# Kernel optimization log

Measured on AMD Instinct MI355X. Metric: run time of the kernel, lower is better.

## Reference

```python
import jax, jax.numpy as jnp
import numpy as np

MAX_REL = 127  # default max_relative_position of NEZHA-style RelativePositionsEncoding


def rel_pos_encoding(L, d):
    """Clipped relative-distance sinusoidal encoding, shape [L, L, d]."""
    vocab = 2 * MAX_REL + 1
    pos = np.arange(vocab, dtype=np.float32)[:, None]
    i = np.arange(d)
    div = np.power(10000.0, (2 * (i // 2)) / d).astype(np.float32)
    ang = pos / div
    table = np.where(i % 2 == 0, np.sin(ang), np.cos(ang)).astype(np.float32)  # [vocab, d]
    dist = np.clip(np.arange(L)[None, :] - np.arange(L)[:, None], -MAX_REL, MAX_REL) + MAX_REL
    return jnp.asarray(table[dist])  # [L, L, d]


def setup_inputs() -> dict:
    key = jax.random.key(0)
    ks = jax.random.split(key, 5)
    B, L, H, C = 2, 256, 256, 5
    return {
        "hidden_state": jax.random.normal(ks[0], (B, L, H), dtype=jnp.float32),
        "mask": jnp.ones((B, L), dtype=jnp.int32),
        "Wh_w": jax.random.normal(ks[1], (4 * H, H), dtype=jnp.float32) * 0.02,
        "Wh_b": jax.random.normal(ks[2], (H,), dtype=jnp.float32) * 0.02,
        "Wo_w": jax.random.normal(ks[3], (H, C), dtype=jnp.float32) * 0.02,
        "Wo_b": jax.random.normal(ks[4], (C,), dtype=jnp.float32) * 0.02,
    }


def reference(hidden_state, mask, Wh_w, Wh_b, Wo_w, Wo_b):
    B, L, H = hidden_state.shape
    # Decompose Wh over the concat [end, start, end-start, end*start]:
    # Wh(cat) = end@(We+Wd) + start@(Ws-Wd) + (end*start)@Wm + rel@Wh + b  (exact, linearity)
    We, Ws, Wd, Wm = jnp.split(Wh_w, 4, axis=0)  # each [H, H]
    rel = rel_pos_encoding(L, 4 * H)                        # [L, L, 4H]
    rel_term = jnp.einsum('ijk,kh->ijh', rel, Wh_w)         # [L, L, H]
    a = hidden_state @ (We + Wd)                            # end-index contribution  [B, L, H]
    b = hidden_state @ (Ws - Wd)                            # start-index contribution [B, L, H]
    prod = hidden_state[:, :, None, :] * hidden_state[:, None, :, :]  # [B, L, L, H]
    pre = a[:, :, None, :] + b[:, None, :, :] + prod @ Wm + rel_term[None] + Wh_b
    hij = jnp.tanh(pre)                                     # [B, L, L, H]
    logits = hij @ Wo_w + Wo_b                              # [B, L, L, C]
    logits = jnp.transpose(logits, (0, 3, 1, 2))            # [B, C, L, L]
    m = mask.astype(bool)
    bad = (~m[:, None, :, None]) | (~m[:, None, None, :])
    logits = jnp.where(bad, -jnp.inf, logits)
    tri = jnp.tril(jnp.ones((L, L), logits.dtype), -1) * 1e12
    return logits - tri
```

## Files before the change

kernel.cpp:

```cpp
#include <hip/hip_runtime.h>
#include <math.h>

typedef _Float16 half8 __attribute__((ext_vector_type(8)));
typedef _Float16 half4v __attribute__((ext_vector_type(4)));
typedef float floatx4 __attribute__((ext_vector_type(4)));

union U16 { uint4 u; half8 h; };

__global__ __launch_bounds__(256) void k_prep1(
    const float* __restrict__ hs, const float* __restrict__ Wh,
    const float* __restrict__ Wo,
    float* __restrict__ Rp, float* __restrict__ ap, float* __restrict__ bp,
    uint4* __restrict__ WmT2, uint4* __restrict__ WoPk)
{
  __shared__ __align__(16) char pool[32768];
  int bid = blockIdx.x, tid = threadIdx.x;

  if (bid < 256) {
    float (*tbl)[8] = (float(*)[8])pool;
    int dg = bid >> 3, kq = bid & 7, d0 = dg * 8, k0 = kq * 128;
    for (int idx = tid; idx < 1024; idx += 256) {
      int t = idx >> 3, dl = idx & 7;
      int k = k0 + t;
      float e = (float)(k & ~1) * (1.0f / 1024.f);
      float div = powf(10000.f, e);
      float ang = (float)(d0 + dl) / div;
      tbl[t][dl] = (k & 1) ? cosf(ang) : sinf(ang);
    }
    __syncthreads();
    int h = tid;
    float acc[8] = {0, 0, 0, 0, 0, 0, 0, 0};
    for (int kk = 0; kk < 128; ++kk) {
      float wv = Wh[(k0 + kk) * 256 + h];
      float tr[8];
      *(float4*)&tr[0] = *(const float4*)&tbl[kk][0];
      *(float4*)&tr[4] = *(const float4*)&tbl[kk][4];
#pragma unroll
      for (int dl = 0; dl < 8; ++dl) acc[dl] = fmaf(tr[dl], wv, acc[dl]);
    }
#pragma unroll
    for (int dl = 0; dl < 8; ++dl)
      Rp[kq * 65536 + (d0 + dl) * 256 + h] = acc[dl];

  } else if (bid < 512) {
    float (*xs)[8] = (float(*)[8])pool;
    int g = bid - 256, rg = g >> 2, kq = g & 3;
    int r0 = rg * 8, k0 = kq * 64;
    for (int idx = tid; idx < 512; idx += 256) {
      int kk = idx >> 3, r = idx & 7;
      xs[kk][r] = hs[(r0 + r) * 256 + k0 + kk];
    }
    __syncthreads();
    int h = tid;
    float aa[8] = {0, 0, 0, 0, 0, 0, 0, 0}, bb[8] = {0, 0, 0, 0, 0, 0, 0, 0};
    for (int kk = 0; kk < 64; ++kk) {
      int k = k0 + kk;
      float we = Wh[k * 256 + h];
      float wsv = Wh[(256 + k) * 256 + h];
      float wd = Wh[(512 + k) * 256 + h];
      float wA = we + wd, wB = wsv - wd;
      float xr[8];
      *(float4*)&xr[0] = *(const float4*)&xs[kk][0];
      *(float4*)&xr[4] = *(const float4*)&xs[kk][4];
#pragma unroll
      for (int r = 0; r < 8; ++r) {
        aa[r] = fmaf(xr[r], wA, aa[r]);
        bb[r] = fmaf(xr[r], wB, bb[r]);
      }
    }
#pragma unroll
    for (int r = 0; r < 8; ++r) {
      ap[kq * 131072 + (r0 + r) * 256 + h] = aa[r];
      bp[kq * 131072 + (r0 + r) * 256 + h] = bb[r];
    }

  } else if (bid < 516) {
    _Float16 (*T)[256] = (_Float16(*)[256])pool;
    int q = bid - 512;
    for (int idx = tid; idx < 16384; idx += 256) {
      int k = idx >> 8, h = idx & 255;
      T[k][h] = (_Float16)Wh[(768 + q * 64 + k) * 256 + h];
    }
    __syncthreads();
    for (int gi = tid; gi < 2048; gi += 256) {
      int kbl = gi >> 8, h = gi & 255;
      U16 v;
#pragma unroll
      for (int e = 0; e < 8; ++e) v.h[e] = T[kbl * 8 + e][h];
      WmT2[(q * 8 + kbl) * 256 + h] = v.u;
    }

  } else {
    for (int gi = tid; gi < 512; gi += 256) {
      int kb = gi >> 4, c = gi & 15;
      U16 v;
#pragma unroll
      for (int e = 0; e < 8; ++e)
        v.h[e] = (c < 5) ? (_Float16)Wo[(kb * 8 + e) * 5 + c] : (_Float16)0.f;
      WoPk[gi] = v.u;
    }
  }
}

__global__ __launch_bounds__(256) void k_prep2(
    const float* __restrict__ Rp, const float* __restrict__ ap,
    const float* __restrict__ bp,
    float* __restrict__ R, float* __restrict__ a, float* __restrict__ bv)
{
  int bid = blockIdx.x, h = threadIdx.x;
  if (bid < 255) {
    int d = bid;
    float s = 0.f;
#pragma unroll
    for (int kq = 0; kq < 8; ++kq) s += Rp[kq * 65536 + d * 256 + h];
    R[d * 256 + h] = s;
  } else {
    int r0 = (bid - 255) * 2;
#pragma unroll
    for (int rr = 0; rr < 2; ++rr) {
      int r = r0 + rr;
      float sa = 0.f, sb = 0.f;
#pragma unroll
      for (int kq = 0; kq < 4; ++kq) {
        sa += ap[kq * 131072 + r * 256 + h];
        sb += bp[kq * 131072 + r * 256 + h];
      }
      a[r * 256 + h] = sa;
      bv[r * 256 + h] = sb;
    }
  }
}

__global__ __launch_bounds__(256, 5) void k_main(
    const float* __restrict__ hs, const int* __restrict__ mask,
    const float* __restrict__ R, const float* __restrict__ a,
    const float* __restrict__ bvec, const float* __restrict__ Whb,
    const uint4* __restrict__ WmT2, const uint4* __restrict__ WoPk,
    const float* __restrict__ Wob, float* __restrict__ out)
{
  __shared__ __align__(16) _Float16 As[32][264];

  int bid = blockIdx.x, tid = threadIdx.x;
  int jt = bid & 7, i = (bid >> 3) & 255, b = bid >> 11;
  int j0 = jt * 32;
  int lane = tid & 63, w = tid >> 6;
  int c16 = lane & 15, quad = lane >> 4;
  const float* hsb = hs + (size_t)b * 65536;

  float av[4];
#pragma unroll
  for (int ht2 = 0; ht2 < 4; ++ht2) {
    int hp = 64 * w + 16 * ht2 + c16;
    av[ht2] = a[((size_t)(b * 256 + i)) * 256 + hp] + Whb[hp];
  }
  floatx4 acc[2][4];
#pragma unroll
  for (int jt2 = 0; jt2 < 2; ++jt2) {
#pragma unroll
    for (int r = 0; r < 4; ++r) {
      int jl = jt2 * 16 + quad * 4 + r;
      int jg = j0 + jl;
      int dd = jg - i;
      dd = dd < -127 ? -127 : (dd > 127 ? 127 : dd);
      dd += 127;
      const float* bpr = bvec + ((size_t)(b * 256 + jg)) * 256;
      const float* rpr = R + (size_t)dd * 256;
#pragma unroll
      for (int ht2 = 0; ht2 < 4; ++ht2) {
        int hp = 64 * w + 16 * ht2 + c16;
        acc[jt2][ht2][r] = av[ht2] + bpr[hp] + rpr[hp];
      }
    }
  }

  for (int idx = tid; idx < 1024; idx += 256) {
    int j = idx >> 5, k8 = (idx & 31) * 8;
    float4 xi0 = *(const float4*)(hsb + i * 256 + k8);
    float4 xi1 = *(const float4*)(hsb + i * 256 + k8 + 4);
    float4 xj0 = *(const float4*)(hsb + (j0 + j) * 256 + k8);
    float4 xj1 = *(const float4*)(hsb + (j0 + j) * 256 + k8 + 4);
    half8 p = {(_Float16)(xi0.x * xj0.x), (_Float16)(xi0.y * xj0.y),
               (_Float16)(xi0.z * xj0.z), (_Float16)(xi0.w * xj0.w),
               (_Float16)(xi1.x * xj1.x), (_Float16)(xi1.y * xj1.y),
               (_Float16)(xi1.z * xj1.z), (_Float16)(xi1.w * xj1.w)};
    *(half8*)(&As[j][k8]) = p;
  }
  __syncthreads();

#pragma unroll 1
  for (int kc = 0; kc < 4; ++kc) {
#pragma unroll
    for (int ks = 0; ks < 2; ++ks) {
      int kb = kc * 8 + ks * 4 + quad;
      U16 bg[4];
#pragma unroll
      for (int ht2 = 0; ht2 < 4; ++ht2)
        bg[ht2].u = WmT2[kb * 256 + 64 * w + 16 * ht2 + c16];
      half8 af[2];
#pragma unroll
      for (int jt2 = 0; jt2 < 2; ++jt2)
        af[jt2] = *(const half8*)(&As[jt2 * 16 + c16][kc * 64 + ks * 32 + quad * 8]);
#pragma unroll
      for (int jt2 = 0; jt2 < 2; ++jt2)
#pragma unroll
        for (int ht2 = 0; ht2 < 4; ++ht2)
          acc[jt2][ht2] = __builtin_amdgcn_mfma_f32_16x16x32_f16(
              af[jt2], bg[ht2].h, acc[jt2][ht2], 0, 0, 0);
    }
  }

  __syncthreads();

#pragma unroll
  for (int jt2 = 0; jt2 < 2; ++jt2) {
#pragma unroll
    for (int ht2 = 0; ht2 < 4; ++ht2) {
      int hp = 64 * w + 16 * ht2 + c16;
#pragma unroll
      for (int r = 0; r < 4; ++r) {
        int jl = jt2 * 16 + quad * 4 + r;
        float x = acc[jt2][ht2][r];
        float t = 1.f - 2.f / (__expf(2.f * x) + 1.f);
        As[jl][hp] = (_Float16)t;
      }
    }
  }
  __syncthreads();

  if (w < 2) {
    U16 wog[8];
#pragma unroll
    for (int s = 0; s < 8; ++s) wog[s].u = WoPk[(s * 4 + quad) * 16 + c16];
    floatx4 accE = {0.f, 0.f, 0.f, 0.f};
#pragma unroll
    for (int s = 0; s < 8; ++s) {
      half8 ae = *(const half8*)(&As[16 * w + c16][s * 32 + quad * 8]);
      accE = __builtin_amdgcn_mfma_f32_16x16x32_f16(ae, wog[s].h, accE, 0, 0, 0);
    }
    const int* mb = mask + b * 256;
    int mi = mb[i];
    float wob = (c16 < 5) ? Wob[c16] : 0.f;
#pragma unroll
    for (int r = 0; r < 4; ++r) {
      int jg = j0 + 16 * w + quad * 4 + r;
      float v = accE[r] + wob;
      if (!(mi && mb[jg])) v = -INFINITY;
      if (jg < i) v -= 1e12f;
      if (c16 < 5) out[(((size_t)b * 5 + c16) * 256 + i) * 256 + jg] = v;
    }
  }
}

extern "C" void kernel_launch(void* const* d_in, const int* in_sizes, int n_in,
                              void* d_out, int out_size, void* d_ws, size_t ws_size,
                              hipStream_t stream) {
  const float* hs   = (const float*)d_in[0];
  const int*   mask = (const int*)d_in[1];
  const float* Wh_w = (const float*)d_in[2];
  const float* Wh_b = (const float*)d_in[3];
  const float* Wo_w = (const float*)d_in[4];
  const float* Wo_b = (const float*)d_in[5];

  char* ws = (char*)d_ws;
  float* R    = (float*)(ws + 0);
  float* a    = (float*)(ws + 262144);
  float* bv   = (float*)(ws + 786432);
  uint4* WmT2 = (uint4*)(ws + 1310720);
  uint4* WoPk = (uint4*)(ws + 1441792);
  float* Rp   = (float*)(ws + 1449984);
  float* ap   = (float*)(ws + 3547136);
  float* bp   = (float*)(ws + 5644288);

  k_prep1<<<517, 256, 0, stream>>>(hs, Wh_w, Wo_w, Rp, ap, bp, WmT2, WoPk);
  k_prep2<<<511, 256, 0, stream>>>(Rp, ap, bp, R, a, bv);
  k_main<<<4096, 256, 0, stream>>>(hs, mask, R, a, bv, Wh_b, WmT2, WoPk, Wo_b,
                                   (float*)d_out);
}
```

Measured before the change: 125.4 us.

## Process two query rows per block and fuse prep reduction into one kernel

The main kernel now handles two i rows per block, so each Wm fragment loaded from global memory feeds twice as many MFMAs. The block count is halved and all four waves now take part in the output projection. The two prep kernels are merged into one: split-K partial sums are reduced in shared memory instead of through workspace and a second launch, and the bias is folded into a. The cost is more accumulator registers (occupancy hint drops from 5 to 3) and a prep stage with far fewer, longer-running blocks.

```diff
diff --git a/kernel.cpp b/kernel.cpp
--- a/kernel.cpp
+++ b/kernel.cpp
@@ -2,87 +2,104 @@
 #include <math.h>
 
 typedef _Float16 half8 __attribute__((ext_vector_type(8)));
-typedef _Float16 half4v __attribute__((ext_vector_type(4)));
 typedef float floatx4 __attribute__((ext_vector_type(4)));
 
 union U16 { uint4 u; half8 h; };
 
-__global__ __launch_bounds__(256) void k_prep1(
+__global__ __launch_bounds__(512) void k_prep(
     const float* __restrict__ hs, const float* __restrict__ Wh,
-    const float* __restrict__ Wo,
-    float* __restrict__ Rp, float* __restrict__ ap, float* __restrict__ bp,
+    const float* __restrict__ Whb, const float* __restrict__ Wo,
+    float* __restrict__ R, float* __restrict__ a, float* __restrict__ bv,
     uint4* __restrict__ WmT2, uint4* __restrict__ WoPk)
 {
   __shared__ __align__(16) char pool[32768];
   int bid = blockIdx.x, tid = threadIdx.x;
 
-  if (bid < 256) {
-    float (*tbl)[8] = (float(*)[8])pool;
-    int dg = bid >> 3, kq = bid & 7, d0 = dg * 8, k0 = kq * 128;
-    for (int idx = tid; idx < 1024; idx += 256) {
-      int t = idx >> 3, dl = idx & 7;
-      int k = k0 + t;
+  if (bid < 64) {
+    float (*tbl)[4] = (float(*)[4])pool;
+    float* part = (float*)(pool + 16384);
+    int d0 = bid * 4;
+    for (int idx = tid; idx < 4096; idx += 512) {
+      int k = idx >> 2, dl = idx & 3;
       float e = (float)(k & ~1) * (1.0f / 1024.f);
       float div = powf(10000.f, e);
       float ang = (float)(d0 + dl) / div;
-      tbl[t][dl] = (k & 1) ? cosf(ang) : sinf(ang);
-    }
-    __syncthreads();
-    int h = tid;
-    float acc[8] = {0, 0, 0, 0, 0, 0, 0, 0};
+      tbl[k][dl] = (k & 1) ? cosf(ang) : sinf(ang);
+    }
+    __syncthreads();
+    int h = tid & 255, s = tid >> 8;
+    float acc[4] = {0.f, 0.f, 0.f, 0.f};
+    for (int kk = 0; kk < 512; ++kk) {
+      int k = s * 512 + kk;
+      float wv = Wh[k * 256 + h];
+      float4 tr = *(const float4*)&tbl[k][0];
+      acc[0] = fmaf(tr.x, wv, acc[0]);
+      acc[1] = fmaf(tr.y, wv, acc[1]);
+      acc[2] = fmaf(tr.z, wv, acc[2]);
+      acc[3] = fmaf(tr.w, wv, acc[3]);
+    }
+    if (s) {
+#pragma unroll
+      for (int dl = 0; dl < 4; ++dl) part[dl * 256 + h] = acc[dl];
+    }
+    __syncthreads();
+    if (!s) {
+#pragma unroll
+      for (int dl = 0; dl < 4; ++dl)
+        if (d0 + dl < 255)
+          R[(d0 + dl) * 256 + h] = acc[dl] + part[dl * 256 + h];
+    }
+
+  } else if (bid < 128) {
+    float (*xs)[8] = (float(*)[8])pool;
+    float* pa = (float*)(pool + 8192);
+    float* pb = (float*)(pool + 16384);
+    int r0 = (bid - 64) * 8;
+    for (int idx = tid; idx < 2048; idx += 512) {
+      int k = idx & 255, r = idx >> 8;
+      xs[k][r] = hs[(r0 + r) * 256 + k];
+    }
+    __syncthreads();
+    int h = tid & 255, s = tid >> 8;
+    float aa[8] = {0, 0, 0, 0, 0, 0, 0, 0}, bb[8] = {0, 0, 0, 0, 0, 0, 0, 0};
     for (int kk = 0; kk < 128; ++kk) {
-      float wv = Wh[(k0 + kk) * 256 + h];
-      float tr[8];
-      *(float4*)&tr[0] = *(const float4*)&tbl[kk][0];
-      *(float4*)&tr[4] = *(const float4*)&tbl[kk][4];
-#pragma unroll
-      for (int dl = 0; dl < 8; ++dl) acc[dl] = fmaf(tr[dl], wv, acc[dl]);
-    }
-#pragma unroll
-    for (int dl = 0; dl < 8; ++dl)
-      Rp[kq * 65536 + (d0 + dl) * 256 + h] = acc[dl];
-
-  } else if (bid < 512) {
-    float (*xs)[8] = (float(*)[8])pool;
-    int g = bid - 256, rg = g >> 2, kq = g & 3;
-    int r0 = rg * 8, k0 = kq * 64;
-    for (int idx = tid; idx < 512; idx += 256) {
-      int kk = idx >> 3, r = idx & 7;
-      xs[kk][r] = hs[(r0 + r) * 256 + k0 + kk];
-    }
-    __syncthreads();
-    int h = tid;
-    float aa[8] = {0, 0, 0, 0, 0, 0, 0, 0}, bb[8] = {0, 0, 0, 0, 0, 0, 0, 0};
-    for (int kk = 0; kk < 64; ++kk) {
-      int k = k0 + kk;
+      int k = s * 128 + kk;
       float we = Wh[k * 256 + h];
       float wsv = Wh[(256 + k) * 256 + h];
       float wd = Wh[(512 + k) * 256 + h];
       float wA = we + wd, wB = wsv - wd;
       float xr[8];
-      *(float4*)&xr[0] = *(const float4*)&xs[kk][0];
-      *(float4*)&xr[4] = *(const float4*)&xs[kk][4];
+      *(float4*)&xr[0] = *(const float4*)&xs[k][0];
+      *(float4*)&xr[4] = *(const float4*)&xs[k][4];
 #pragma unroll
       for (int r = 0; r < 8; ++r) {
         aa[r] = fmaf(xr[r], wA, aa[r]);
         bb[r] = fmaf(xr[r], wB, bb[r]);
       }
     }
-#pragma unroll
-    for (int r = 0; r < 8; ++r) {
-      ap[kq * 131072 + (r0 + r) * 256 + h] = aa[r];
-      bp[kq * 131072 + (r0 + r) * 256 + h] = bb[r];
-    }
-
-  } else if (bid < 516) {
+    if (s) {
+#pragma unroll
+      for (int r = 0; r < 8; ++r) { pa[r * 256 + h] = aa[r]; pb[r * 256 + h] = bb[r]; }
+    }
+    __syncthreads();
+    if (!s) {
+      float bias = Whb[h];
+#pragma unroll
+      for (int r = 0; r < 8; ++r) {
+        a[(r0 + r) * 256 + h] = aa[r] + pa[r * 256 + h] + bias;
+        bv[(r0 + r) * 256 + h] = bb[r] + pb[r * 256 + h];
+      }
+    }
+
+  } else if (bid < 132) {
     _Float16 (*T)[256] = (_Float16(*)[256])pool;
-    int q = bid - 512;
-    for (int idx = tid; idx < 16384; idx += 256) {
+    int q = bid - 128;
+    for (int idx = tid; idx < 16384; idx += 512) {
       int k = idx >> 8, h = idx & 255;
       T[k][h] = (_Float16)Wh[(768 + q * 64 + k) * 256 + h];
     }
     __syncthreads();
-    for (int gi = tid; gi < 2048; gi += 256) {
+    for (int gi = tid; gi < 2048; gi += 512) {
       int kbl = gi >> 8, h = gi & 255;
       U16 v;
 #pragma unroll
@@ -91,7 +108,7 @@
     }
 
   } else {
-    for (int gi = tid; gi < 512; gi += 256) {
+    for (int gi = tid; gi < 512; gi += 512) {
       int kb = gi >> 4, c = gi & 15;
       U16 v;
 #pragma unroll
@@ -102,88 +119,63 @@
   }
 }
 
-__global__ __launch_bounds__(256) void k_prep2(
-    const float* __restrict__ Rp, const float* __restrict__ ap,
-    const float* __restrict__ bp,
-    float* __restrict__ R, float* __restrict__ a, float* __restrict__ bv)
-{
-  int bid = blockIdx.x, h = threadIdx.x;
-  if (bid < 255) {
-    int d = bid;
-    float s = 0.f;
-#pragma unroll
-    for (int kq = 0; kq < 8; ++kq) s += Rp[kq * 65536 + d * 256 + h];
-    R[d * 256 + h] = s;
-  } else {
-    int r0 = (bid - 255) * 2;
-#pragma unroll
-    for (int rr = 0; rr < 2; ++rr) {
-      int r = r0 + rr;
-      float sa = 0.f, sb = 0.f;
-#pragma unroll
-      for (int kq = 0; kq < 4; ++kq) {
-        sa += ap[kq * 131072 + r * 256 + h];
-        sb += bp[kq * 131072 + r * 256 + h];
-      }
-      a[r * 256 + h] = sa;
-      bv[r * 256 + h] = sb;
-    }
-  }
-}
-
-__global__ __launch_bounds__(256, 5) void k_main(
+__global__ __launch_bounds__(256, 3) void k_main(
     const float* __restrict__ hs, const int* __restrict__ mask,
     const float* __restrict__ R, const float* __restrict__ a,
-    const float* __restrict__ bvec, const float* __restrict__ Whb,
-    const uint4* __restrict__ WmT2, const uint4* __restrict__ WoPk,
-    const float* __restrict__ Wob, float* __restrict__ out)
+    const float* __restrict__ bvec, const uint4* __restrict__ WmT2,
+    const uint4* __restrict__ WoPk, const float* __restrict__ Wob,
+    float* __restrict__ out)
 {
-  __shared__ __align__(16) _Float16 As[32][264];
+  __shared__ __align__(16) _Float16 As[2][32][264];
 
   int bid = blockIdx.x, tid = threadIdx.x;
-  int jt = bid & 7, i = (bid >> 3) & 255, b = bid >> 11;
-  int j0 = jt * 32;
+  int jt = bid & 7, ig = (bid >> 3) & 127, b = bid >> 10;
+  int i0 = ig * 2, j0 = jt * 32;
   int lane = tid & 63, w = tid >> 6;
   int c16 = lane & 15, quad = lane >> 4;
   const float* hsb = hs + (size_t)b * 65536;
 
-  float av[4];
-#pragma unroll
-  for (int ht2 = 0; ht2 < 4; ++ht2) {
-    int hp = 64 * w + 16 * ht2 + c16;
-    av[ht2] = a[((size_t)(b * 256 + i)) * 256 + hp] + Whb[hp];
-  }
-  floatx4 acc[2][4];
+  float av[2][4];
+#pragma unroll
+  for (int i2 = 0; i2 < 2; ++i2)
+#pragma unroll
+    for (int ht2 = 0; ht2 < 4; ++ht2)
+      av[i2][ht2] = a[((size_t)(b * 256 + i0 + i2)) * 256 + 64 * w + 16 * ht2 + c16];
+
+  floatx4 acc[2][2][4];
 #pragma unroll
   for (int jt2 = 0; jt2 < 2; ++jt2) {
 #pragma unroll
     for (int r = 0; r < 4; ++r) {
-      int jl = jt2 * 16 + quad * 4 + r;
-      int jg = j0 + jl;
-      int dd = jg - i;
-      dd = dd < -127 ? -127 : (dd > 127 ? 127 : dd);
-      dd += 127;
-      const float* bpr = bvec + ((size_t)(b * 256 + jg)) * 256;
-      const float* rpr = R + (size_t)dd * 256;
-#pragma unroll
-      for (int ht2 = 0; ht2 < 4; ++ht2) {
-        int hp = 64 * w + 16 * ht2 + c16;
-        acc[jt2][ht2][r] = av[ht2] + bpr[hp] + rpr[hp];
-      }
-    }
-  }
-
-  for (int idx = tid; idx < 1024; idx += 256) {
-    int j = idx >> 5, k8 = (idx & 31) * 8;
-    float4 xi0 = *(const float4*)(hsb + i * 256 + k8);
-    float4 xi1 = *(const float4*)(hsb + i * 256 + k8 + 4);
+      int jg = j0 + jt2 * 16 + quad * 4 + r;
+      float bvv[4];
+#pragma unroll
+      for (int ht2 = 0; ht2 < 4; ++ht2)
+        bvv[ht2] = bvec[((size_t)(b * 256 + jg)) * 256 + 64 * w + 16 * ht2 + c16];
+#pragma unroll
+      for (int i2 = 0; i2 < 2; ++i2) {
+        int dd = jg - (i0 + i2);
+        dd = dd < -127 ? -127 : (dd > 127 ? 127 : dd);
+        dd += 127;
+        const float* rp = R + (size_t)dd * 256 + 64 * w;
+#pragma unroll
+        for (int ht2 = 0; ht2 < 4; ++ht2)
+          acc[i2][jt2][ht2][r] = av[i2][ht2] + bvv[ht2] + rp[16 * ht2 + c16];
+      }
+    }
+  }
+
+  for (int idx = tid; idx < 2048; idx += 256) {
+    int i2 = idx >> 10, j = (idx >> 5) & 31, k8 = (idx & 31) * 8;
+    float4 xi0 = *(const float4*)(hsb + (i0 + i2) * 256 + k8);
+    float4 xi1 = *(const float4*)(hsb + (i0 + i2) * 256 + k8 + 4);
     float4 xj0 = *(const float4*)(hsb + (j0 + j) * 256 + k8);
     float4 xj1 = *(const float4*)(hsb + (j0 + j) * 256 + k8 + 4);
     half8 p = {(_Float16)(xi0.x * xj0.x), (_Float16)(xi0.y * xj0.y),
                (_Float16)(xi0.z * xj0.z), (_Float16)(xi0.w * xj0.w),
                (_Float16)(xi1.x * xj1.x), (_Float16)(xi1.y * xj1.y),
                (_Float16)(xi1.z * xj1.z), (_Float16)(xi1.w * xj1.w)};
-    *(half8*)(&As[j][k8]) = p;
+    *(half8*)(&As[i2][j][k8]) = p;
   }
   __syncthreads();
 
@@ -196,58 +188,65 @@
 #pragma unroll
       for (int ht2 = 0; ht2 < 4; ++ht2)
         bg[ht2].u = WmT2[kb * 256 + 64 * w + 16 * ht2 + c16];
-      half8 af[2];
-#pragma unroll
-      for (int jt2 = 0; jt2 < 2; ++jt2)
-        af[jt2] = *(const half8*)(&As[jt2 * 16 + c16][kc * 64 + ks * 32 + quad * 8]);
-#pragma unroll
-      for (int jt2 = 0; jt2 < 2; ++jt2)
-#pragma unroll
-        for (int ht2 = 0; ht2 < 4; ++ht2)
-          acc[jt2][ht2] = __builtin_amdgcn_mfma_f32_16x16x32_f16(
-              af[jt2], bg[ht2].h, acc[jt2][ht2], 0, 0, 0);
+      half8 af[2][2];
+#pragma unroll
+      for (int i2 = 0; i2 < 2; ++i2)
+#pragma unroll
+        for (int jt2 = 0; jt2 < 2; ++jt2)
+          af[i2][jt2] =
+              *(const half8*)(&As[i2][jt2 * 16 + c16][kc * 64 + ks * 32 + quad * 8]);
+#pragma unroll
+      for (int i2 = 0; i2 < 2; ++i2)
+#pragma unroll
+        for (int jt2 = 0; jt2 < 2; ++jt2)
+#pragma unroll
+          for (int ht2 = 0; ht2 < 4; ++ht2)
+            acc[i2][jt2][ht2] = __builtin_amdgcn_mfma_f32_16x16x32_f16(
+                af[i2][jt2], bg[ht2].h, acc[i2][jt2][ht2], 0, 0, 0);
     }
   }
 
   __syncthreads();
 
 #pragma unroll
-  for (int jt2 = 0; jt2 < 2; ++jt2) {
-#pragma unroll
-    for (int ht2 = 0; ht2 < 4; ++ht2) {
-      int hp = 64 * w + 16 * ht2 + c16;
-#pragma unroll
-      for (int r = 0; r < 4; ++r) {
-        int jl = jt2 * 16 + quad * 4 + r;
-        float x = acc[jt2][ht2][r];
-        float t = 1.f - 2.f / (__expf(2.f * x) + 1.f);
-        As[jl][hp] = (_Float16)t;
-      }
-    }
-  }
+  for (int i2 = 0; i2 < 2; ++i2)
+#pragma unroll
+    for (int jt2 = 0; jt2 < 2; ++jt2)
+#pragma unroll
+      for (int ht2 = 0; ht2 < 4; ++ht2) {
+        int hp = 64 * w + 16 * ht2 + c16;
+#pragma unroll
+        for (int r = 0; r < 4; ++r) {
+          int jl = jt2 * 16 + quad * 4 + r;
+          float x = acc[i2][jt2][ht2][r];
+          float t = 1.f - 2.f / (__expf(2.f * x) + 1.f);
+          As[i2][jl][hp] = (_Float16)t;
+        }
+      }
   __syncthreads();
 
-  if (w < 2) {
-    U16 wog[8];
-#pragma unroll
-    for (int s = 0; s < 8; ++s) wog[s].u = WoPk[(s * 4 + quad) * 16 + c16];
-    floatx4 accE = {0.f, 0.f, 0.f, 0.f};
-#pragma unroll
-    for (int s = 0; s < 8; ++s) {
-      half8 ae = *(const half8*)(&As[16 * w + c16][s * 32 + quad * 8]);
-      accE = __builtin_amdgcn_mfma_f32_16x16x32_f16(ae, wog[s].h, accE, 0, 0, 0);
-    }
-    const int* mb = mask + b * 256;
-    int mi = mb[i];
-    float wob = (c16 < 5) ? Wob[c16] : 0.f;
-#pragma unroll
-    for (int r = 0; r < 4; ++r) {
-      int jg = j0 + 16 * w + quad * 4 + r;
-      float v = accE[r] + wob;
-      if (!(mi && mb[jg])) v = -INFINITY;
-      if (jg < i) v -= 1e12f;
-      if (c16 < 5) out[(((size_t)b * 5 + c16) * 256 + i) * 256 + jg] = v;
-    }
+  U16 wog[8];
+#pragma unroll
+  for (int s = 0; s < 8; ++s) wog[s].u = WoPk[(s * 4 + quad) * 16 + c16];
+  floatx4 accE = {0.f, 0.f, 0.f, 0.f};
+  int arow = 16 * w + c16;
+  int i2a = arow >> 5, jla = arow & 31;
+#pragma unroll
+  for (int s = 0; s < 8; ++s) {
+    half8 ae = *(const half8*)(&As[i2a][jla][s * 32 + quad * 8]);
+    accE = __builtin_amdgcn_mfma_f32_16x16x32_f16(ae, wog[s].h, accE, 0, 0, 0);
+  }
+
+  const int* mb = mask + b * 256;
+  float wob = (c16 < 5) ? Wob[c16] : 0.f;
+#pragma unroll
+  for (int r = 0; r < 4; ++r) {
+    int grow = 16 * w + quad * 4 + r;
+    int ii = i0 + (grow >> 5), jg = j0 + (grow & 31);
+    float v = accE[r] + wob;
+    if (!(mb[ii] && mb[jg])) v = -INFINITY;
+    if (jg < ii) v -= 1e12f;
+    if (c16 < 5) out[(((size_t)b * 5 + c16) * 256 + ii) * 256 + jg] = v;
   }
 }
 
@@ -267,12 +266,8 @@
   float* bv   = (float*)(ws + 786432);
   uint4* WmT2 = (uint4*)(ws + 1310720);
   uint4* WoPk = (uint4*)(ws + 1441792);
-  float* Rp   = (float*)(ws + 1449984);
-  float* ap   = (float*)(ws + 3547136);
-  float* bp   = (float*)(ws + 5644288);
-
-  k_prep1<<<517, 256, 0, stream>>>(hs, Wh_w, Wo_w, Rp, ap, bp, WmT2, WoPk);
-  k_prep2<<<511, 256, 0, stream>>>(Rp, ap, bp, R, a, bv);
-  k_main<<<4096, 256, 0, stream>>>(hs, mask, R, a, bv, Wh_b, WmT2, WoPk, Wo_b,
+
+  k_prep<<<133, 512, 0, stream>>>(hs, Wh_w, Wh_b, Wo_w, R, a, bv, WmT2, WoPk);
+  k_main<<<2048, 256, 0, stream>>>(hs, mask, R, a, bv, WmT2, WoPk, Wo_b,
                                    (float*)d_out);
 }
```

After: 131.8 us. +5.1%, slower.
